# Kernel optimization log

Hardware: AMD Instinct MI355X
Metric: run time of the kernel (lower is better)

Reference implementation:

```python
import jax, jax.numpy as jnp
import numpy as np

B, T, H, W, C = 2, 8, 20, 36, 512
NH = 4
HD = C // NH
WS = (5, 9)
EXP = (2, 4)              # window_size // 2
KP = (5, 9)               # focal unfold kernel for level k=0
PADP = (2, 4)
T2T_K, T2T_S, T2T_P = (7, 7), (3, 3), (3, 3)
FFN_HD = 1960
NWH, NWW = H // WS[0], W // WS[1]   # 4, 4
WAREA = WS[0] * WS[1]               # 45


def _valid_ind_rolled():
    wh, ww = WS
    eh, ew = EXP
    m = np.ones((4, wh, ww), np.float32)
    m[0, :wh - eh, :ww - ew] = 0   # tl
    m[1, :wh - eh, ew:] = 0        # tr
    m[2, eh:, :ww - ew] = 0        # bl
    m[3, eh:, ew:] = 0             # br
    return jnp.asarray(np.nonzero(m.reshape(-1))[0])

VALID_ROLLED = _valid_ind_rolled()  # (120,)


def unfold(x, k, s, p):
    # x: (N, Cc, Hh, Ww) -> (N, Cc*kh*kw, L); matches torch.nn.Unfold layout (c slowest).
    N, Cc, Hh, Ww = x.shape
    kh, kw = k; sh, sw = s; ph, pw = p
    xp = jnp.pad(x, ((0, 0), (0, 0), (ph, ph), (pw, pw)))
    oh = (Hh + 2 * ph - kh) // sh + 1
    ow = (Ww + 2 * pw - kw) // sw + 1
    cols = [xp[:, :, i:i + oh * sh:sh, j:j + ow * sw:sw]
            for i in range(kh) for j in range(kw)]
    patches = jnp.stack(cols, axis=2)            # (N, Cc, kh*kw, oh, ow)
    return patches.reshape(N, Cc * kh * kw, oh * ow)


def fold(patches, out_hw, k, s, p):
    # inverse of unfold (overlap-add), matches torch F.fold.
    N = patches.shape[0]
    kh, kw = k; sh, sw = s; ph, pw = p
    Hh, Ww = out_hw
    oh = (Hh + 2 * ph - kh) // sh + 1
    ow = (Ww + 2 * pw - kw) // sw + 1
    Cc = patches.shape[1] // (kh * kw)
    pr = patches.reshape(N, Cc, kh, kw, oh, ow)
    out = jnp.zeros((N, Cc, Hh + 2 * ph, Ww + 2 * pw), patches.dtype)
    for i in range(kh):
        for j in range(kw):
            out = out.at[:, :, i:i + oh * sh:sh, j:j + ow * sw:sw].add(pr[:, :, i, j])
    return out[:, :, ph:ph + Hh, pw:pw + Ww]


def layer_norm(x, g, b):
    mu = jnp.mean(x, -1, keepdims=True)
    var = jnp.var(x, -1, keepdims=True)
    return (x - mu) * jax.lax.rsqrt(var + 1e-5) * g + b


def win_part(x):
    # (B,T,H,W,C) -> (B*nW, T*wh*ww, C)
    b = x.shape[0]
    x = x.reshape(b, T, NWH, WS[0], NWW, WS[1], C)
    return x.transpose(0, 2, 4, 1, 3, 5, 6).reshape(-1, T * WAREA, C)


def to_heads(w):
    return w.reshape(-1, T, WAREA, NH, HD).transpose(0, 3, 1, 2, 4).reshape(-1, NH, T * WAREA, HD)


def block_forward(x, g1, be1, wqkv, bqkv, wproj, bproj, wpool, bpool, g2, be2, w1, bf1, w2, bf2, out_h, out_w):
    shortcut = x
    xn = layer_norm(x, g1, be1)

    # ---- coarser (pooled) focal level, k=0 (focal_level=2) ----
    wnr = xn.reshape(B, T, NWH, WS[0], NWW, WS[1], C).transpose(0, 2, 4, 1, 3, 5, 6)
    wnr = wnr.reshape(B, NWH, NWW, T, WAREA, C)
    pooled = jnp.einsum('bhwtnc,n->bhwtc', wnr, wpool) + bpool   # (B,NWH,NWW,T,C)

    # ---- window attention ----
    qkv = xn @ wqkv + bqkv                                       # (B,T,H,W,3C)
    q, k, v = jnp.split(qkv, 3, axis=-1)
    qw = to_heads(win_part(q)) * (HD ** -0.5)
    kw_, vw = to_heads(win_part(k)), to_heads(win_part(v))

    def rolled(t):
        parts = []
        for sh, sw in ((-EXP[0], -EXP[1]), (-EXP[0], EXP[1]), (EXP[0], -EXP[1]), (EXP[0], EXP[1])):
            r = jnp.roll(t, (sh, sw), axis=(2, 3))
            parts.append(win_part(r).reshape(-1, T, WAREA, NH, HD))
        cat = jnp.concatenate(parts, axis=2)                     # (B*nW, T, 4*warea, NH, HD)
        cat = jnp.take(cat.transpose(0, 3, 1, 2, 4), VALID_ROLLED, axis=3)
        return cat.reshape(-1, NH, T * VALID_ROLLED.shape[0], HD)

    k_rolled = jnp.concatenate([kw_, rolled(k)], axis=2)         # (B*nW, NH, T*165, HD)
    v_rolled = jnp.concatenate([vw, rolled(v)], axis=2)

    # pooled keys/values via focal unfold
    xp = pooled.transpose(0, 3, 1, 2, 4)                          # (B,T,NWH,NWW,C)
    qkv_p = xp @ wqkv + bqkv
    kp, vp = qkv_p[..., C:2 * C], qkv_p[..., 2 * C:]

    def unfold_kv(t):
        t = t.transpose(0, 1, 4, 2, 3).reshape(B * T, C, NWH, NWW)
        u = unfold(t, KP, (1, 1), PADP)                           # (B*T, C*45, L)
        L = u.shape[-1]
        u = u.reshape(B, T, C, KP[0], KP[1], L).transpose(0, 5, 1, 3, 4, 2)
        u = u.reshape(B * L, T, KP[0] * KP[1], NH, HD).transpose(0, 3, 1, 2, 4)
        return u.reshape(B * L, NH, T * KP[0] * KP[1], HD)

    k_all = jnp.concatenate([k_rolled, unfold_kv(kp)], axis=2)
    v_all = jnp.concatenate([v_rolled, unfold_kv(vp)], axis=2)

    attn = jnp.einsum('wnqd,wnkd->wnqk', qw, k_all)               # (B*nW, NH, T*45, N)

    # validity mask for pooled context (zero-padded unfold positions -> -100)
    ones = jnp.ones((T, 1, NWH, NWW), x.dtype)
    um = unfold(ones, KP, (1, 1), PADP)                           # (T, 45, L)
    L = um.shape[-1]
    mvals = jnp.where(um.reshape(T, KP[0] * KP[1], L).transpose(2, 0, 1).reshape(L, -1) == 0,
                      jnp.asarray(-100.0, x.dtype), jnp.asarray(0.0, x.dtype))
    n_rolled = k_rolled.shape[2]
    mask_cols = jnp.concatenate([jnp.zeros((L, n_rolled), x.dtype), mvals], axis=1)
    attn = attn + jnp.tile(mask_cols, (B, 1))[:, None, None, :]

    attn = jax.nn.softmax(attn, axis=-1)
    out = jnp.einsum('wnqk,wnkd->wnqd', attn, v_all)
    out = out.transpose(0, 2, 1, 3).reshape(-1, T * WAREA, C) @ wproj + bproj

    # window reverse + residual
    out = out.reshape(B, NWH, NWW, T, WS[0], WS[1], C)
    out = out.transpose(0, 3, 1, 4, 2, 5, 6).reshape(B, T, H, W, C)
    x = shortcut + out

    # ---- FusionFeedForward (fold/unfold re-normalized MLP) ----
    y = layer_norm(x, g2, be2).reshape(B, T * H * W, C)
    h = y @ w1 + bf1                                              # (B, n, 1960)
    nvec = ((out_h + 2 * T2T_P[0] - T2T_K[0]) // T2T_S[0] + 1) * \
           ((out_w + 2 * T2T_P[1] - T2T_K[1]) // T2T_S[1] + 1)
    bt = (B * T * H * W) // nvec
    norm_p = jnp.ones((bt, T2T_K[0] * T2T_K[1], nvec), x.dtype)
    norm_f = fold(norm_p, (out_h, out_w), T2T_K, T2T_S, T2T_P)    # (bt,1,out_h,out_w)
    h_f = fold(h.reshape(bt, nvec, FFN_HD).transpose(0, 2, 1), (out_h, out_w), T2T_K, T2T_S, T2T_P)
    h = unfold(h_f / norm_f, T2T_K, T2T_S, T2T_P).transpose(0, 2, 1).reshape(B, T * H * W, FFN_HD)
    h = jax.nn.gelu(h, approximate=False) @ w2 + bf2
    return x + h.reshape(B, T, H, W, C)


def setup_inputs() -> dict:
    key = jax.random.key(0)
    ks = jax.random.split(key, 8)
    s = 0.02
    return dict(
        x=jax.random.normal(ks[0], (B, T, H, W, C), jnp.float32),
        g1=jnp.ones((C,), jnp.float32),
        be1=jnp.zeros((C,), jnp.float32),
        wqkv=jax.random.normal(ks[1], (C, 3 * C), jnp.float32) * s,
        bqkv=jnp.zeros((3 * C,), jnp.float32),
        wproj=jax.random.normal(ks[2], (C, C), jnp.float32) * s,
        bproj=jnp.zeros((C,), jnp.float32),
        wpool=jnp.full((WAREA,), 1.0 / WAREA, jnp.float32),
        bpool=jnp.zeros((1,), jnp.float32),
        g2=jnp.ones((C,), jnp.float32),
        be2=jnp.zeros((C,), jnp.float32),
        w1=jax.random.normal(ks[3], (C, FFN_HD), jnp.float32) * s,
        bf1=jnp.zeros((FFN_HD,), jnp.float32),
        w2=jax.random.normal(ks[4], (FFN_HD, C), jnp.float32) * s,
        bf2=jnp.zeros((C,), jnp.float32),
        out_h=60,
        out_w=108,
    )


def reference(x, g1, be1, wqkv, bqkv, wproj, bproj, wpool, bpool, g2, be2, w1, bf1, w2, bf2, out_h, out_w):
    return block_forward(x, g1, be1, wqkv, bqkv, wproj, bproj, wpool, bpool,
                         g2, be2, w1, bf1, w2, bf2, out_h, out_w)
```

## Files before the change

### kernel.cpp

```cpp
#include <hip/hip_runtime.h>
#include <hip/hip_bf16.h>
#include <math.h>

typedef __hip_bfloat16 bf16;
typedef __attribute__((ext_vector_type(8))) short bf16x8;
typedef __attribute__((ext_vector_type(4))) float f32x4;

#define DEVI __device__ __forceinline__

#define C_ 512
#define NH_ 4
#define NTOK 11520
#define NKEY 1680
#define NRK 120
#define FFN_ 1960
#define ZROW (NTOK + 256)

DEVI float ldf(const bf16* p) { return __bfloat162float(*p); }
DEVI float ldf(const float* p) { return *p; }
DEVI void stw(bf16* p, float v) { *p = __float2bfloat16(v); }
DEVI void stw(float* p, float v) { *p = v; }
DEVI unsigned short f2bs(float f) { bf16 h = __float2bfloat16(f); return *(unsigned short*)&h; }

template <int DT> DEVI float ldw(const void* p, size_t i) {
  if (DT == 0) return __bfloat162float(((const bf16*)p)[i]);
  else         return ((const float*)p)[i];
}

DEVI void gload_lds16(const void* g, void* l) {
  __builtin_amdgcn_global_load_lds(
      (const __attribute__((address_space(1))) void*)g,
      (__attribute__((address_space(3))) void*)l, 16, 0, 0);
}

__global__ void k_init(const void* __restrict__ g1, int* __restrict__ flag,
                       int* __restrict__ table, bf16* __restrict__ zp) {
  if (blockIdx.x == 0) {
    if (threadIdx.x == 0) {
      const unsigned short* p = (const unsigned short*)g1;
      *flag = (p[0] == 0x3F80u) ? 0 : 1;
      int cnt = 0;
      for (int pq = 0; pq < 4; pq++)
        for (int wi = 0; wi < 5; wi++)
          for (int wj = 0; wj < 9; wj++) {
            bool invalid;
            if (pq == 0)      invalid = (wi < 3) && (wj < 5);
            else if (pq == 1) invalid = (wi < 3) && (wj >= 4);
            else if (pq == 2) invalid = (wi >= 2) && (wj < 5);
            else              invalid = (wi >= 2) && (wj >= 4);
            if (!invalid) table[cnt++] = pq * 45 + wi * 9 + wj;
          }
    }
  } else {
    zp[(blockIdx.x - 1) * 256 + threadIdx.x] = __float2bfloat16(0.f);
  }
}

__global__ void k_ksrc(const int* __restrict__ vtab, int* __restrict__ ksrc) {
  int idx = blockIdx.x * 256 + threadIdx.x;
  if (idx >= 32 * NKEY) return;
  int w = idx / NKEY, j = idx % NKEY;
  int b = w >> 4, nh = (w >> 2) & 3, nw = w & 3;
  int val;
  if (j < 360) {
    int t = j / 45, pos = j % 45, wi = pos / 9, wj2 = pos % 9;
    val = ((b * 8 + t) * 20 + nh * 5 + wi) * 36 + nw * 9 + wj2;
  } else if (j < 1320) {
    int jj = j - 360;
    int t = jj / 120, r = jj % 120;
    int id = vtab[r];
    int p = id / 45, pos = id % 45, wi = pos / 9, wj2 = pos % 9;
    int sh = (p < 2) ? -2 : 2;
    int sw = (p & 1) ? 4 : -4;
    int hh = nh * 5 + wi - sh;
    if (hh < 0) hh += 20; else if (hh >= 20) hh -= 20;
    int ww2 = nw * 9 + wj2 - sw;
    if (ww2 < 0) ww2 += 36; else if (ww2 >= 36) ww2 -= 36;
    val = ((b * 8 + t) * 20 + hh) * 36 + ww2;
  } else {
    int jj = j - 1320;
    int t = jj / 45, kidx = jj % 45, ki = kidx / 9, kj = kidx % 9;
    int snh = nh + ki - 2, snw = nw + kj - 4;
    if (snh < 0 || snh >= 4 || snw < 0 || snw >= 4) val = -1;
    else val = NTOK + (b * 8 + t) * 16 + snh * 4 + snw;
  }
  ksrc[idx] = val;
}

template <int DT>
DEVI void wcvt_body(const void* in, bf16* out, int K, int N, int Npad) {
  __shared__ float t[64][65];
  const int n0 = blockIdx.x * 64;
  const int k0 = blockIdx.y * 64;
  const int tx = threadIdx.x & 63, tg = threadIdx.x >> 6;
#pragma unroll
  for (int r = 0; r < 16; r++) {
    int k = k0 + r * 4 + tg;
    int nn = n0 + tx;
    float v = (k < K && nn < N) ? ldw<DT>(in, (size_t)k * N + nn) : 0.f;
    t[r * 4 + tg][tx] = v;
  }
  __syncthreads();
#pragma unroll
  for (int r = 0; r < 16; r++) {
    int nn = n0 + r * 4 + tg;
    int k = k0 + tx;
    if (nn < Npad && k < K)
      out[(size_t)nn * K + k] = __float2bfloat16(t[tx][r * 4 + tg]);
  }
}
__global__ void k_wcvt(const int* __restrict__ dflag, const void* __restrict__ in,
                       bf16* __restrict__ out, int K, int N, int Npad) {
  if (*dflag == 0) wcvt_body<0>(in, out, K, N, Npad);
  else             wcvt_body<1>(in, out, K, N, Npad);
}

__global__ void k_bcvt4(const int* __restrict__ dflag,
                        const void* __restrict__ b0, float* __restrict__ o0,
                        const void* __restrict__ b1, float* __restrict__ o1,
                        const void* __restrict__ b2, float* __restrict__ o2,
                        const void* __restrict__ b3, float* __restrict__ o3) {
  int dt = *dflag;
  int bx = blockIdx.x;
  const void* src; float* dst; int n, i;
  if (bx < 6)       { src = b0; dst = o0; n = 1536; i = bx * 256 + threadIdx.x; }
  else if (bx < 8)  { src = b1; dst = o1; n = 512;  i = (bx - 6) * 256 + threadIdx.x; }
  else if (bx < 16) { src = b2; dst = o2; n = FFN_; i = (bx - 8) * 256 + threadIdx.x; }
  else              { src = b3; dst = o3; n = 512;  i = (bx - 16) * 256 + threadIdx.x; }
  if (i < n) dst[i] = (dt == 0) ? ldw<0>(src, i) : ldw<1>(src, i);
}

template <int DTIN, int DTP>
DEVI void ln_body(const void* xin, const void* g, const void* be, bf16* out) {
  const int tok = blockIdx.x;
  const int tid = threadIdx.x;
  const size_t base = (size_t)tok * C_;
  float v0 = ldw<DTIN>(xin, base + tid);
  float v1 = ldw<DTIN>(xin, base + tid + 256);
  float s = v0 + v1, ss = v0 * v0 + v1 * v1;
#pragma unroll
  for (int o = 32; o; o >>= 1) { s += __shfl_xor(s, o); ss += __shfl_xor(ss, o); }
  __shared__ float sh[10];
  const int lane = tid & 63, wv = tid >> 6;
  if (lane == 0) { sh[wv] = s; sh[4 + wv] = ss; }
  __syncthreads();
  if (tid == 0) {
    float a = sh[0] + sh[1] + sh[2] + sh[3];
    float q = sh[4] + sh[5] + sh[6] + sh[7];
    float mu = a * (1.0f / C_);
    float var = q * (1.0f / C_) - mu * mu;
    sh[8] = mu; sh[9] = rsqrtf(fmaxf(var, 0.f) + 1e-5f);
  }
  __syncthreads();
  float mu = sh[8], inv = sh[9];
  stw(out + base + tid,
      (v0 - mu) * inv * ldw<DTP>(g, tid) + ldw<DTP>(be, tid));
  stw(out + base + tid + 256,
      (v1 - mu) * inv * ldw<DTP>(g, tid + 256) + ldw<DTP>(be, tid + 256));
}
__global__ void k_ln(const int* __restrict__ dflag, int mode,
                     const void* __restrict__ xin, const void* __restrict__ g,
                     const void* __restrict__ be, bf16* __restrict__ out) {
  int dt = *dflag;
  if (mode == 0) {
    if (dt == 0) ln_body<0, 0>(xin, g, be, out);
    else         ln_body<1, 1>(xin, g, be, out);
  } else {
    if (dt == 0) ln_body<1, 0>(xin, g, be, out);
    else         ln_body<1, 1>(xin, g, be, out);
  }
}

template <int DT>
DEVI void pool_body(const bf16* xn, const void* wpool, const void* bpool,
                    float* pooled) {
  int idx = blockIdx.x * blockDim.x + threadIdx.x;
  if (idx >= 256 * C_) return;
  int c = idx & (C_ - 1);
  int fw = idx >> 9;
  int nw = fw & 3, nh = (fw >> 2) & 3;
  int bt = fw >> 4;
  float acc = ldw<DT>(bpool, 0);
  for (int wi = 0; wi < 5; wi++) {
    int hh = nh * 5 + wi;
    const bf16* base = xn + (((size_t)(bt * 20 + hh)) * 36 + nw * 9) * C_ + c;
    for (int wj = 0; wj < 9; wj++)
      acc += __bfloat162float(base[(size_t)wj * C_]) * ldw<DT>(wpool, wi * 9 + wj);
  }
  pooled[idx] = acc;
}
__global__ void k_pool(const int* __restrict__ dflag, const bf16* __restrict__ xn,
                       const void* __restrict__ wpool, const void* __restrict__ bpool,
                       float* __restrict__ pooled) {
  if (*dflag == 0) pool_body<0>(xn, wpool, bpool, pooled);
  else             pool_body<1>(xn, wpool, bpool, pooled);
}

template <int DT>
DEVI void gemm_small_body(const float* A, const void* Bw, const void* bias,
                          bf16* Cc) {
  __shared__ float As[8][512];
  const int n = blockIdx.x * 256 + threadIdx.x;
  const int m0 = blockIdx.y * 8;
  for (int i = threadIdx.x; i < 8 * 512; i += 256)
    As[i >> 9][i & 511] = A[(size_t)(m0 + (i >> 9)) * 512 + (i & 511)];
  __syncthreads();
  float acc[8];
  float bv = ldw<DT>(bias, n);
#pragma unroll
  for (int mm = 0; mm < 8; mm++) acc[mm] = bv;
  for (int k = 0; k < 512; k++) {
    float b = ldw<DT>(Bw, (size_t)k * 1536 + n);
#pragma unroll
    for (int mm = 0; mm < 8; mm++) acc[mm] += As[mm][k] * b;
  }
#pragma unroll
  for (int mm = 0; mm < 8; mm++)
    Cc[(size_t)(m0 + mm) * 1536 + n] = __float2bfloat16(acc[mm]);
}
__global__ void k_gemm_small(const int* __restrict__ dflag, const float* __restrict__ A,
                             const void* __restrict__ Bw, const void* __restrict__ bias,
                             bf16* __restrict__ Cc) {
  if (*dflag == 0) gemm_small_body<0>(A, Bw, bias, Cc);
  else             gemm_small_body<1>(A, Bw, bias, Cc);
}

template <int RES>
__global__ __launch_bounds__(256) void k_gemm_m(const int* __restrict__ dflag,
                                                const bf16* __restrict__ A,
                                                const bf16* __restrict__ Bt,
                                                const float* __restrict__ bias,
                                                const void* __restrict__ resid,
                                                void* __restrict__ out,
                                                int M, int N, int K) {
  const int dt = dflag ? *dflag : 0;
  __shared__ __align__(16) unsigned short As[2][128 * 32];
  __shared__ __align__(16) unsigned short Bs[2][128 * 32];
  const int tid = threadIdx.x;
  const int lane = tid & 63, wid = tid >> 6;
  const int r15 = lane & 15, quad = lane >> 4;
  const int wm = wid >> 1, wn = wid & 1;
  const int nbx = gridDim.x;
  const int lin = blockIdx.x + nbx * blockIdx.y;
  const int cpx = (nbx * gridDim.y) >> 3;
  const int swz = (lin & 7) * cpx + (lin >> 3);
  const int m0 = (swz / nbx) * 128, n0 = (swz % nbx) * 128;

  f32x4 acc[4][4];
#pragma unroll
  for (int i = 0; i < 4; i++)
#pragma unroll
    for (int j = 0; j < 4; j++)
#pragma unroll
      for (int e = 0; e < 4; e++) acc[i][j][e] = 0.f;

  const int lrow = lane >> 2, lcol = (lane & 3) * 8;

  for (int k0 = 0; k0 < K; k0 += 64) {
    int rem = K - k0;
    if (rem >= 64) {
      const bf16* ga = A + (size_t)(m0 + wid * 32 + lrow) * K + k0 + lcol;
      gload_lds16(ga, &As[0][wid * 1024]);
      gload_lds16(ga + (size_t)16 * K, &As[0][wid * 1024 + 512]);
      gload_lds16(ga + 32, &As[1][wid * 1024]);
      gload_lds16(ga + (size_t)16 * K + 32, &As[1][wid * 1024 + 512]);
      const bf16* gb = Bt + (size_t)(n0 + wid * 32 + lrow) * K + k0 + lcol;
      gload_lds16(gb, &Bs[0][wid * 1024]);
      gload_lds16(gb + (size_t)16 * K, &Bs[0][wid * 1024 + 512]);
      gload_lds16(gb + 32, &Bs[1][wid * 1024]);
      gload_lds16(gb + (size_t)16 * K + 32, &Bs[1][wid * 1024 + 512]);
    } else {
      int r = tid >> 3, c = (tid & 7) * 8;
      uint4 z = make_uint4(0, 0, 0, 0);
      int h = c >> 5, cc = c & 31;
#pragma unroll
      for (int p = 0; p < 4; p++) {
        int row = r + p * 32;
        uint4 av = z, bv = z;
        if (c < rem) {
          av = *(const uint4*)(A + (size_t)(m0 + row) * K + k0 + c);
          bv = *(const uint4*)(Bt + (size_t)(n0 + row) * K + k0 + c);
        }
        *(uint4*)&As[h][row * 32 + cc] = av;
        *(uint4*)&Bs[h][row * 32 + cc] = bv;
      }
    }
    __syncthreads();

#pragma unroll
    for (int h = 0; h < 2; h++) {
      bf16x8 af[4], bfr[4];
#pragma unroll
      for (int mf = 0; mf < 4; mf++)
        af[mf] = *(const bf16x8*)&As[h][(wm * 64 + mf * 16 + r15) * 32 + quad * 8];
#pragma unroll
      for (int nf = 0; nf < 4; nf++)
        bfr[nf] = *(const bf16x8*)&Bs[h][(wn * 64 + nf * 16 + r15) * 32 + quad * 8];
#pragma unroll
      for (int mf = 0; mf < 4; mf++)
#pragma unroll
        for (int nf = 0; nf < 4; nf++)
          acc[mf][nf] = __builtin_amdgcn_mfma_f32_16x16x32_bf16(af[mf], bfr[nf],
                                                                acc[mf][nf], 0, 0, 0);
    }
    __syncthreads();
  }

#pragma unroll
  for (int nf = 0; nf < 4; nf++) {
    int n = n0 + wn * 64 + nf * 16 + r15;
    if (n >= N) continue;
    float bv = bias[n];
#pragma unroll
    for (int mf = 0; mf < 4; mf++) {
      int mb = m0 + wm * 64 + mf * 16 + quad * 4;
#pragma unroll
      for (int e = 0; e < 4; e++) {
        size_t off = (size_t)(mb + e) * N + n;
        float v = acc[mf][nf][e] + bv;
        if (RES == 1) v += (dt == 0) ? ldw<0>(resid, off) : ldw<1>(resid, off);
        else if (RES == 2) v += ((const float*)resid)[off];
        if (RES == 0) ((bf16*)out)[off] = __float2bfloat16(v);
        else if (RES == 1) ((float*)out)[off] = v;
        else {
          if (dt == 0) ((bf16*)out)[off] = __float2bfloat16(v);
          else         ((float*)out)[off] = v;
        }
      }
    }
  }
}

#define KT 64
#define KPAD 136
#define VPAD 72
__global__ __launch_bounds__(768) void k_attn_m(const bf16* __restrict__ qkv,
                                                const int* __restrict__ ksrc,
                                                bf16* __restrict__ ao) {
  __shared__ int ks_l[NKEY];
  __shared__ __align__(16) unsigned short ktl[2][KT * KPAD];
  __shared__ __align__(16) unsigned short vtl[2][128 * VPAD];
  __shared__ __align__(16) unsigned short ptl[12 * 16 * VPAD];
  __shared__ float maskv[2][KT];

  const int tid = threadIdx.x;
  const int lane = tid & 63, wid = tid >> 6;
  const int r15 = lane & 15, quad = lane >> 4;
  const int w = blockIdx.x, qt = blockIdx.y, n = blockIdx.z;
  const int b = w >> 4, nh = (w >> 2) & 3, nw = w & 3;
  const unsigned short* qkvs = (const unsigned short*)qkv;

  for (int j = tid; j < NKEY; j += 768) ks_l[j] = ksrc[w * NKEY + j];

  bf16x8 qf[4];
  {
    int qw = qt * 192 + wid * 16 + r15;
    int qc2 = qw < 360 ? qw : 359;
    int t = qc2 / 45, pos = qc2 % 45, wi = pos / 9, wj = pos % 9;
    int tok = ((b * 8 + t) * 20 + nh * 5 + wi) * 36 + nw * 9 + wj;
    const unsigned short* qp = qkvs + (size_t)tok * 1536 + n * 128 + quad * 8;
#pragma unroll
    for (int c = 0; c < 4; c++)
      qf[c] = *(const bf16x8*)(qp + c * 32);
  }

  f32x4 of[8];
#pragma unroll
  for (int nt = 0; nt < 8; nt++)
#pragma unroll
    for (int e = 0; e < 4; e++) of[nt][e] = 0.f;
  float m_[4], l_[4];
#pragma unroll
  for (int e = 0; e < 4; e++) { m_[e] = -1e30f; l_[e] = 0.f; }

  unsigned short* ptw = &ptl[wid * 16 * VPAD];

  const bool isK = (wid < 4);
  const int kr = tid >> 2, kp = tid & 3;
  const int vr = lane, vp8 = wid - 4;
  uint4 k0, k1, k2, k3, v0, v1;
  float mreg = -30000.f;
  const unsigned short* kbase = qkvs + 512 + n * 128 + kp * 32;
  const unsigned short* vbase = qkvs + 1024 + n * 128 + vp8 * 16;

  auto load_tile = [&](int j0) {
    int cnt = NKEY - j0; if (cnt > KT) cnt = KT;
    if (isK) {
      int s0 = (kr < cnt) ? ks_l[j0 + kr] : -1;
      mreg = (s0 < 0) ? -30000.f : 0.f;
      int row = (s0 < 0) ? ZROW : s0;
      const uint4* kq = (const uint4*)(kbase + (size_t)row * 1536);
      k0 = kq[0]; k1 = kq[1]; k2 = kq[2]; k3 = kq[3];
    } else {
      int s1 = (vr < cnt) ? ks_l[j0 + vr] : -1;
      int row = (s1 < 0) ? ZROW : s1;
      const uint4* vq = (const uint4*)(vbase + (size_t)row * 1536);
      v0 = vq[0]; v1 = vq[1];
    }
  };

  auto store_tile = [&](int buf) {
    if (isK) {
      if (kp == 0) maskv[buf][kr] = mreg;
      unsigned short* kb = &ktl[buf][kr * KPAD + kp * 32];
      *(uint4*)&kb[0]  = k0;
      *(uint4*)&kb[8]  = k1;
      *(uint4*)&kb[16] = k2;
      *(uint4*)&kb[24] = k3;
    } else {
      unsigned short* vb = &vtl[buf][0];
      int d0 = vp8 * 16;
      vb[(d0 + 0) * VPAD + vr]  = (unsigned short)(v0.x & 0xFFFFu);
      vb[(d0 + 1) * VPAD + vr]  = (unsigned short)(v0.x >> 16);
      vb[(d0 + 2) * VPAD + vr]  = (unsigned short)(v0.y & 0xFFFFu);
      vb[(d0 + 3) * VPAD + vr]  = (unsigned short)(v0.y >> 16);
      vb[(d0 + 4) * VPAD + vr]  = (unsigned short)(v0.z & 0xFFFFu);
      vb[(d0 + 5) * VPAD + vr]  = (unsigned short)(v0.z >> 16);
      vb[(d0 + 6) * VPAD + vr]  = (unsigned short)(v0.w & 0xFFFFu);
      vb[(d0 + 7) * VPAD + vr]  = (unsigned short)(v0.w >> 16);
      vb[(d0 + 8) * VPAD + vr]  = (unsigned short)(v1.x & 0xFFFFu);
      vb[(d0 + 9) * VPAD + vr]  = (unsigned short)(v1.x >> 16);
      vb[(d0 + 10) * VPAD + vr] = (unsigned short)(v1.y & 0xFFFFu);
      vb[(d0 + 11) * VPAD + vr] = (unsigned short)(v1.y >> 16);
      vb[(d0 + 12) * VPAD + vr] = (unsigned short)(v1.z & 0xFFFFu);
      vb[(d0 + 13) * VPAD + vr] = (unsigned short)(v1.z >> 16);
      vb[(d0 + 14) * VPAD + vr] = (unsigned short)(v1.w & 0xFFFFu);
      vb[(d0 + 15) * VPAD + vr] = (unsigned short)(v1.w >> 16);
    }
  };

  __syncthreads();
  load_tile(0);
  store_tile(0);
  load_tile(KT);
  __syncthreads();

  int cur = 0, j0 = 0;
  while (true) {
    int nxt = j0 + KT;
    if (nxt < NKEY) {
      store_tile(cur ^ 1);
      if (nxt + KT < NKEY) load_tile(nxt + KT);
    }

    const unsigned short* ktc = &ktl[cur][0];
    const unsigned short* vtc = &vtl[cur][0];
    const float* mkc = maskv[cur];

    f32x4 sf[4];
#pragma unroll
    for (int ft = 0; ft < 4; ft++)
#pragma unroll
      for (int e = 0; e < 4; e++) sf[ft][e] = 0.f;
#pragma unroll
    for (int kc = 0; kc < 4; kc++) {
      bf16x8 a = qf[kc];
#pragma unroll
      for (int ft = 0; ft < 4; ft++) {
        bf16x8 bb = *(const bf16x8*)&ktc[(ft * 16 + r15) * KPAD + kc * 32 + quad * 8];
        sf[ft] = __builtin_amdgcn_mfma_f32_16x16x32_bf16(a, bb, sf[ft], 0, 0, 0);
      }
    }
    const float scl = 0.088388347648318447f;
#pragma unroll
    for (int ft = 0; ft < 4; ft++) {
      float mk = mkc[ft * 16 + r15];
#pragma unroll
      for (int e = 0; e < 4; e++) sf[ft][e] = sf[ft][e] * scl + mk;
    }
    float tm[4];
#pragma unroll
    for (int e = 0; e < 4; e++) {
      float v = fmaxf(fmaxf(sf[0][e], sf[1][e]), fmaxf(sf[2][e], sf[3][e]));
#pragma unroll
      for (int o = 1; o < 16; o <<= 1) v = fmaxf(v, __shfl_xor(v, o));
      tm[e] = v;
    }
    bool grow = (tm[0] > m_[0] + 8.f) | (tm[1] > m_[1] + 8.f) |
                (tm[2] > m_[2] + 8.f) | (tm[3] > m_[3] + 8.f);
    if (__any(grow)) {
#pragma unroll
      for (int e = 0; e < 4; e++) {
        float mn = fmaxf(m_[e], tm[e]);
        float alpha = __expf(m_[e] - mn);
        m_[e] = mn;
        float rs = 0.f;
#pragma unroll
        for (int ft = 0; ft < 4; ft++) {
          float pv = __expf(sf[ft][e] - mn);
          rs += pv;
          ptw[(quad * 4 + e) * VPAD + ft * 16 + r15] = f2bs(pv);
        }
        l_[e] = l_[e] * alpha + rs;
#pragma unroll
        for (int nt = 0; nt < 8; nt++) of[nt][e] *= alpha;
      }
    } else {
#pragma unroll
      for (int e = 0; e < 4; e++) {
        float rs = 0.f;
#pragma unroll
        for (int ft = 0; ft < 4; ft++) {
          float pv = __expf(sf[ft][e] - m_[e]);
          rs += pv;
          ptw[(quad * 4 + e) * VPAD + ft * 16 + r15] = f2bs(pv);
        }
        l_[e] += rs;
      }
    }
#pragma unroll
    for (int kc = 0; kc < 2; kc++) {
      bf16x8 pa = *(const bf16x8*)&ptw[r15 * VPAD + kc * 32 + quad * 8];
#pragma unroll
      for (int nt = 0; nt < 8; nt++) {
        bf16x8 vb = *(const bf16x8*)&vtc[(nt * 16 + r15) * VPAD + kc * 32 + quad * 8];
        of[nt] = __builtin_amdgcn_mfma_f32_16x16x32_bf16(pa, vb, of[nt], 0, 0, 0);
      }
    }

    if (nxt >= NKEY) break;
    __syncthreads();
    cur ^= 1; j0 = nxt;
  }

#pragma unroll
  for (int e = 0; e < 4; e++) {
#pragma unroll
    for (int o = 1; o < 16; o <<= 1) l_[e] += __shfl_xor(l_[e], o);
  }
#pragma unroll
  for (int e = 0; e < 4; e++) {
    int qw = qt * 192 + wid * 16 + quad * 4 + e;
    if (qw >= 360) continue;
    float inv = 1.0f / l_[e];
    int t = qw / 45, pos = qw % 45, wi = pos / 9, wj = pos % 9;
    int tok = ((b * 8 + t) * 20 + nh * 5 + wi) * 36 + nw * 9 + wj;
    bf16* op = ao + (size_t)tok * 512 + n * 128 + r15;
#pragma unroll
    for (int nt = 0; nt < 8; nt++)
      stw(op + nt * 16, of[nt][e] * inv);
  }
}

__global__ void k_fold(const bf16* __restrict__ h1, float* __restrict__ hf) {
  int idx = blockIdx.x * 256 + threadIdx.x;
  if (idx >= 16 * 40 * 60 * 108) return;
  int x = idx % 108;
  int tmp = idx / 108;
  int y = tmp % 60; tmp /= 60;
  int c = tmp % 40;
  int bt = tmp / 40;
  float sum = 0.f;
  int cnt = 0;
  for (int ki = y % 3; ki < 7; ki += 3) {
    int num = y + 3 - ki;
    if (num < 0) continue;
    int oh = num / 3;
    if (oh >= 20) continue;
    for (int kj = x % 3; kj < 7; kj += 3) {
      int num2 = x + 3 - kj;
      if (num2 < 0) continue;
      int ow = num2 / 3;
      if (ow >= 36) continue;
      sum += __bfloat162float(
          h1[(size_t)(bt * 720 + oh * 36 + ow) * FFN_ + c * 49 + ki * 7 + kj]);
      cnt++;
    }
  }
  hf[idx] = sum / (float)cnt;
}

__global__ void k_unfold_gelu(const float* __restrict__ hf, bf16* __restrict__ h2) {
  int idx = blockIdx.x * 256 + threadIdx.x;
  if (idx >= NTOK * FFN_) return;
  int f = idx % FFN_;
  int token = idx / FFN_;
  int c = f / 49, k = f % 49, ki = k / 7, kj = k % 7;
  int bt = token / 720, vec = token % 720;
  int oh = vec / 36, ow = vec % 36;
  int y = oh * 3 + ki - 3, x = ow * 3 + kj - 3;
  float v = 0.f;
  if (y >= 0 && y < 60 && x >= 0 && x < 108)
    v = hf[((size_t)(bt * 40 + c) * 60 + y) * 108 + x];
  float g = 0.5f * v * (1.0f + erff(v * 0.70710678118654752f));
  stw(h2 + idx, g);
}

extern "C" void kernel_launch(void* const* d_in, const int* in_sizes, int n_in,
                              void* d_out, int out_size, void* d_ws, size_t ws_size,
                              hipStream_t stream) {
  (void)in_sizes; (void)n_in; (void)out_size; (void)ws_size;
  const void* x     = d_in[0];
  const void* g1    = d_in[1];
  const void* be1   = d_in[2];
  const void* wqkv  = d_in[3];
  const void* bqkv  = d_in[4];
  const void* wproj = d_in[5];
  const void* bproj = d_in[6];
  const void* wpool = d_in[7];
  const void* bpool = d_in[8];
  const void* g2    = d_in[9];
  const void* be2   = d_in[10];
  const void* w1    = d_in[11];
  const void* bf1   = d_in[12];
  const void* w2    = d_in[13];
  const void* bf2   = d_in[14];

  char* ws = (char*)d_ws;
  size_t off = 0;
  auto alloc = [&](size_t bytes) -> void* {
    void* p = ws + off;
    off += (bytes + 255) & ~(size_t)255;
    return p;
  };

  int*   dflag  = (int*)  alloc(256);
  int*   vtab   = (int*)  alloc(NRK * sizeof(int));
  int*   ksrc   = (int*)  alloc((size_t)32 * NKEY * sizeof(int));
  bf16*  buf2   = (bf16*) alloc((size_t)NTOK * FFN_ * 2);
  float* pooled = (float*)alloc((size_t)256 * C_ * 4);
  float* x2     = (float*)alloc((size_t)NTOK * C_ * 4);
  float* hf     = (float*)alloc((size_t)16 * 40 * 60 * 108 * 4);
  bf16*  wqkv_t = (bf16*) alloc((size_t)1536 * 512 * 2);
  bf16*  wproj_t= (bf16*) alloc((size_t)512 * 512 * 2);
  bf16*  w1_t   = (bf16*) alloc((size_t)2048 * 512 * 2);
  bf16*  w2_t   = (bf16*) alloc((size_t)512 * FFN_ * 2);
  float* bqkv_f = (float*)alloc(1536 * 4);
  float* bproj_f= (float*)alloc(512 * 4);
  float* bf1_f  = (float*)alloc(FFN_ * 4);
  float* bf2_f  = (float*)alloc(512 * 4);

  bf16* buf1 = (bf16*)d_out;
  bf16* xn = buf1;
  bf16* ao = buf1;
  bf16* y  = buf1;
  bf16* qkv = buf2;
  bf16* h1  = buf2;
  bf16* qkvpb = buf2 + (size_t)NTOK * 1536;

  k_init<<<7, 256, 0, stream>>>(g1, dflag, vtab, qkvpb + (size_t)256 * 1536);
  k_ksrc<<<(32 * NKEY) / 256, 256, 0, stream>>>(vtab, ksrc);

  k_wcvt<<<dim3(24, 8), 256, 0, stream>>>(dflag, wqkv, wqkv_t, 512, 1536, 1536);
  k_wcvt<<<dim3(8, 8), 256, 0, stream>>>(dflag, wproj, wproj_t, 512, 512, 512);
  k_wcvt<<<dim3(32, 8), 256, 0, stream>>>(dflag, w1, w1_t, 512, FFN_, 2048);
  k_wcvt<<<dim3(8, 31), 256, 0, stream>>>(dflag, w2, w2_t, FFN_, 512, 512);
  k_bcvt4<<<18, 256, 0, stream>>>(dflag, bqkv, bqkv_f, bproj, bproj_f,
                                  bf1, bf1_f, bf2, bf2_f);

  k_ln<<<NTOK, 256, 0, stream>>>(dflag, 0, x, g1, be1, xn);

  k_pool<<<512, 256, 0, stream>>>(dflag, xn, wpool, bpool, pooled);

  k_gemm_m<0><<<dim3(12, 90), 256, 0, stream>>>(
      nullptr, xn, wqkv_t, bqkv_f, nullptr, qkv, NTOK, 1536, 512);

  k_gemm_small<<<dim3(6, 32), 256, 0, stream>>>(dflag, pooled, wqkv, bqkv, qkvpb);

  k_attn_m<<<dim3(32, 2, NH_), 768, 0, stream>>>(qkv, ksrc, ao);

  k_gemm_m<1><<<dim3(4, 90), 256, 0, stream>>>(
      dflag, ao, wproj_t, bproj_f, x, x2, NTOK, 512, 512);

  k_ln<<<NTOK, 256, 0, stream>>>(dflag, 1, x2, g2, be2, y);

  k_gemm_m<0><<<dim3(16, 90), 256, 0, stream>>>(
      nullptr, y, w1_t, bf1_f, nullptr, h1, NTOK, FFN_, 512);

  k_fold<<<(16 * 40 * 60 * 108) / 256, 256, 0, stream>>>(h1, hf);

  k_unfold_gelu<<<(NTOK * FFN_) / 256, 256, 0, stream>>>(hf, h1);

  k_gemm_m<2><<<dim3(4, 90), 256, 0, stream>>>(
      dflag, h1, w2_t, bf2_f, x2, d_out, NTOK, 512, FFN_);
}
```

Before: 542.9 us.

## Add 256x128-tile GEMM with XCD swizzle for QKV/FFN1; merge weight-convert launches

Adds a new bf16 MFMA GEMM kernel with 512 threads and 256x128 output tiles, plus an XCD-aware block swizzle, and uses it for the QKV and first FFN projections. The larger M tile is meant to halve B-tile reloads per output and improve L2 locality across chiplets. Separately, the four weight transpose/convert launches are merged into one 760-block launch to cut launch overhead. The new GEMM loads tiles with no double buffering across k-steps, so latency hiding relies on occupancy, which may drop because of the larger LDS and register footprint.

```diff
diff --git a/kernel.cpp b/kernel.cpp
--- a/kernel.cpp
+++ b/kernel.cpp
@@ -88,10 +88,9 @@
 }
 
 template <int DT>
-DEVI void wcvt_body(const void* in, bf16* out, int K, int N, int Npad) {
+DEVI void wcvt_body(const void* in, bf16* out, int K, int N, int Npad,
+                    int n0, int k0) {
   __shared__ float t[64][65];
-  const int n0 = blockIdx.x * 64;
-  const int k0 = blockIdx.y * 64;
   const int tx = threadIdx.x & 63, tg = threadIdx.x >> 6;
 #pragma unroll
   for (int r = 0; r < 16; r++) {
@@ -109,10 +108,20 @@
       out[(size_t)nn * K + k] = __float2bfloat16(t[tx][r * 4 + tg]);
   }
 }
-__global__ void k_wcvt(const int* __restrict__ dflag, const void* __restrict__ in,
-                       bf16* __restrict__ out, int K, int N, int Npad) {
-  if (*dflag == 0) wcvt_body<0>(in, out, K, N, Npad);
-  else             wcvt_body<1>(in, out, K, N, Npad);
+__global__ void k_wcvt4(const int* __restrict__ dflag,
+                        const void* __restrict__ i0, bf16* __restrict__ o0,
+                        const void* __restrict__ i1, bf16* __restrict__ o1,
+                        const void* __restrict__ i2, bf16* __restrict__ o2,
+                        const void* __restrict__ i3, bf16* __restrict__ o3) {
+  int b = blockIdx.x;
+  const void* in; bf16* out; int K, N, Npad, nb, lb;
+  if (b < 192)      { in = i0; out = o0; K = 512;  N = 1536; Npad = 1536; nb = 24; lb = b; }
+  else if (b < 256) { in = i1; out = o1; K = 512;  N = 512;  Npad = 512;  nb = 8;  lb = b - 192; }
+  else if (b < 512) { in = i2; out = o2; K = 512;  N = FFN_; Npad = 2048; nb = 32; lb = b - 256; }
+  else              { in = i3; out = o3; K = FFN_; N = 512;  Npad = 512;  nb = 8;  lb = b - 512; }
+  int n0 = (lb % nb) * 64, k0 = (lb / nb) * 64;
+  if (*dflag == 0) wcvt_body<0>(in, out, K, N, Npad, n0, k0);
+  else             wcvt_body<1>(in, out, K, N, Npad, n0, k0);
 }
 
 __global__ void k_bcvt4(const int* __restrict__ dflag,
@@ -320,12 +329,87 @@
         float v = acc[mf][nf][e] + bv;
         if (RES == 1) v += (dt == 0) ? ldw<0>(resid, off) : ldw<1>(resid, off);
         else if (RES == 2) v += ((const float*)resid)[off];
-        if (RES == 0) ((bf16*)out)[off] = __float2bfloat16(v);
-        else if (RES == 1) ((float*)out)[off] = v;
+        if (RES == 1) ((float*)out)[off] = v;
         else {
           if (dt == 0) ((bf16*)out)[off] = __float2bfloat16(v);
           else         ((float*)out)[off] = v;
         }
+      }
+    }
+  }
+}
+
+__global__ __launch_bounds__(512) void k_gemm_m2(const bf16* __restrict__ A,
+                                                 const bf16* __restrict__ Bt,
+                                                 const float* __restrict__ bias,
+                                                 bf16* __restrict__ out,
+                                                 int M, int N, int K) {
+  __shared__ __align__(16) unsigned short As[2][256 * 32];
+  __shared__ __align__(16) unsigned short Bs[2][128 * 32];
+  const int tid = threadIdx.x;
+  const int lane = tid & 63, wid = tid >> 6;
+  const int r15 = lane & 15, quad = lane >> 4;
+  const int wm = wid >> 1, wn = wid & 1;
+  const int nbx = gridDim.x;
+  const int nwg = nbx * gridDim.y;
+  const int lin = blockIdx.x + nbx * blockIdx.y;
+  const int q8 = nwg >> 3, r8 = nwg & 7;
+  const int xcd = lin & 7, ii = lin >> 3;
+  const int swz = (xcd < r8 ? xcd * (q8 + 1) : r8 * (q8 + 1) + (xcd - r8) * q8) + ii;
+  const int m0 = (swz / nbx) * 256, n0 = (swz % nbx) * 128;
+
+  f32x4 acc[4][4];
+#pragma unroll
+  for (int i = 0; i < 4; i++)
+#pragma unroll
+    for (int j = 0; j < 4; j++)
+#pragma unroll
+      for (int e = 0; e < 4; e++) acc[i][j][e] = 0.f;
+
+  const int lrow = lane >> 2, lcol = (lane & 3) * 8;
+
+  for (int k0 = 0; k0 < K; k0 += 64) {
+    const bf16* ga = A + (size_t)(m0 + wid * 32 + lrow) * K + k0 + lcol;
+    gload_lds16(ga, &As[0][wid * 1024]);
+    gload_lds16(ga + (size_t)16 * K, &As[0][wid * 1024 + 512]);
+    gload_lds16(ga + 32, &As[1][wid * 1024]);
+    gload_lds16(ga + (size_t)16 * K + 32, &As[1][wid * 1024 + 512]);
+    const bf16* gb = Bt + (size_t)(n0 + wid * 16 + lrow) * K + k0 + lcol;
+    gload_lds16(gb, &Bs[0][wid * 512]);
+    gload_lds16(gb + 32, &Bs[1][wid * 512]);
+    __syncthreads();
+
+#pragma unroll
+    for (int h = 0; h < 2; h++) {
+      bf16x8 af[4], bfr[4];
+#pragma unroll
+      for (int mf = 0; mf < 4; mf++)
+        af[mf] = *(const bf16x8*)&As[h][(wm * 64 + mf * 16 + r15) * 32 + quad * 8];
+#pragma unroll
+      for (int nf = 0; nf < 4; nf++)
+        bfr[nf] = *(const bf16x8*)&Bs[h][(wn * 64 + nf * 16 + r15) * 32 + quad * 8];
+#pragma unroll
+      for (int mf = 0; mf < 4; mf++)
+#pragma unroll
+        for (int nf = 0; nf < 4; nf++)
+          acc[mf][nf] = __builtin_amdgcn_mfma_f32_16x16x32_bf16(af[mf], bfr[nf],
+                                                                acc[mf][nf], 0, 0, 0);
+    }
+    __syncthreads();
+  }
+
+#pragma unroll
+  for (int nf = 0; nf < 4; nf++) {
+    int n = n0 + wn * 64 + nf * 16 + r15;
+    if (n >= N) continue;
+    float bv = bias[n];
+#pragma unroll
+    for (int mf = 0; mf < 4; mf++) {
+      int mb = m0 + wm * 64 + mf * 16 + quad * 4;
+#pragma unroll
+      for (int e = 0; e < 4; e++) {
+        size_t off = (size_t)(mb + e) * N + n;
+        out[off] = __float2bfloat16(acc[mf][nf][e] + bv);
       }
     }
   }
@@ -641,10 +725,8 @@
   k_init<<<7, 256, 0, stream>>>(g1, dflag, vtab, qkvpb + (size_t)256 * 1536);
   k_ksrc<<<(32 * NKEY) / 256, 256, 0, stream>>>(vtab, ksrc);
 
-  k_wcvt<<<dim3(24, 8), 256, 0, stream>>>(dflag, wqkv, wqkv_t, 512, 1536, 1536);
-  k_wcvt<<<dim3(8, 8), 256, 0, stream>>>(dflag, wproj, wproj_t, 512, 512, 512);
-  k_wcvt<<<dim3(32, 8), 256, 0, stream>>>(dflag, w1, w1_t, 512, FFN_, 2048);
-  k_wcvt<<<dim3(8, 31), 256, 0, stream>>>(dflag, w2, w2_t, FFN_, 512, 512);
+  k_wcvt4<<<760, 256, 0, stream>>>(dflag, wqkv, wqkv_t, wproj, wproj_t,
+                                   w1, w1_t, w2, w2_t);
   k_bcvt4<<<18, 256, 0, stream>>>(dflag, bqkv, bqkv_f, bproj, bproj_f,
                                   bf1, bf1_f, bf2, bf2_f);
 
@@ -652,8 +734,8 @@
 
   k_pool<<<512, 256, 0, stream>>>(dflag, xn, wpool, bpool, pooled);
 
-  k_gemm_m<0><<<dim3(12, 90), 256, 0, stream>>>(
-      nullptr, xn, wqkv_t, bqkv_f, nullptr, qkv, NTOK, 1536, 512);
+  k_gemm_m2<<<dim3(12, 45), 512, 0, stream>>>(
+      xn, wqkv_t, bqkv_f, qkv, NTOK, 1536, 512);
 
   k_gemm_small<<<dim3(6, 32), 256, 0, stream>>>(dflag, pooled, wqkv, bqkv, qkvpb);
 
@@ -664,8 +746,8 @@
 
   k_ln<<<NTOK, 256, 0, stream>>>(dflag, 1, x2, g2, be2, y);
 
-  k_gemm_m<0><<<dim3(16, 90), 256, 0, stream>>>(
-      nullptr, y, w1_t, bf1_f, nullptr, h1, NTOK, FFN_, 512);
+  k_gemm_m2<<<dim3(16, 45), 512, 0, stream>>>(
+      y, w1_t, bf1_f, h1, NTOK, FFN_, 512);
 
   k_fold<<<(16 * 40 * 60 * 108) / 256, 256, 0, stream>>>(h1, hf);
 
```

Measured after the change: 535.8 us. No clear change (-1.3%).
